# Optimization experiments

Hardware: AMD Instinct MI355X
Metric: run time of the kernel (lower is better)

The kernel has to match this reference:

```python
import jax, jax.numpy as jnp
import numpy as np

B, S, D, H, DOUT = 4, 2048, 1024, 4, 1024


def setup_inputs() -> dict:
    key = jax.random.key(0)
    ks = jax.random.split(key, 11)
    x = jax.random.normal(ks[0], (B, S, D), dtype=jnp.float32)
    phase = jax.random.normal(ks[1], (H, D), dtype=jnp.float32) * 0.02
    sc = 1.0 / np.sqrt(D)
    Wq = jax.random.normal(ks[2], (D, H * D), dtype=jnp.float32) * sc
    bq = jnp.zeros((H * D,), dtype=jnp.float32)
    Wk = jax.random.normal(ks[3], (D, H * D), dtype=jnp.float32) * sc
    bk = jnp.zeros((H * D,), dtype=jnp.float32)
    Wv = jax.random.normal(ks[4], (D, H * D), dtype=jnp.float32) * sc
    bv = jnp.zeros((H * D,), dtype=jnp.float32)
    Wo = jax.random.normal(ks[5], (H * D, DOUT), dtype=jnp.float32) / np.sqrt(H * D)
    bo = jnp.zeros((DOUT,), dtype=jnp.float32)
    return {"x": x, "phase": phase, "Wq": Wq, "bq": bq, "Wk": Wk, "bk": bk,
            "Wv": Wv, "bv": bv, "Wo": Wo, "bo": bo}


def reference(x, phase, Wq, bq, Wk, bk, Wv, bv, Wo, bo):
    b, s, d = x.shape
    h = phase.shape[0]
    q = (x @ Wq + bq).reshape(b, s, h, d)  # [B,S,H,D]
    k = (x @ Wk + bk).reshape(b, s, h, d)
    v = (x @ Wv + bv).reshape(b, s, h, d)
    # q *= e^{i phase}; k *= e^{-i phase}; scores = Re(q @ k^T) over last dim.
    # Re( e^{i p1} e^{-i p2} ) = cos(p1)cos(p2) + sin(p1)sin(p2), so use real pairs.
    c, sn = jnp.cos(phase), jnp.sin(phase)  # [H,D]
    qr, qi = q * c, q * sn
    kr, ki = k * c, k * sn
    scale = 1.0 / np.sqrt(d)
    # per-position head-vs-head scores: [B,S,H,H]
    scores = (jnp.einsum('bshd,bsgd->bshg', qr, kr)
              + jnp.einsum('bshd,bsgd->bshg', qi, ki)) * scale
    attn = jax.nn.softmax(scores, axis=-1)  # dropout is identity in eval
    out = jnp.einsum('bshg,bsgd->bshd', attn, v)  # [B,S,H,D]
    # replicate torch: transpose(1,2) -> [B,H,S,D] then view [B,S,H*D]
    out = jnp.swapaxes(out, 1, 2).reshape(b, s, h * d)
    return out @ Wo + bo
```

## Files before the change

### kernel.cpp

```cpp
#include <hip/hip_runtime.h>
#include <hip/hip_bf16.h>
#include <stdint.h>

#define DEVI __device__ __forceinline__

using f32x4  = __attribute__((ext_vector_type(4))) float;
using bf16x8 = __attribute__((ext_vector_type(8))) short;

DEVI ushort f2bf(float f) {
  union { float f; uint32_t u; } v; v.f = f;
  uint32_t u = v.u;
  uint32_t r = (u + 0x7fffu + ((u >> 16) & 1u)) >> 16;
  return (ushort)r;
}
DEVI float bf2f(ushort h) {
  union { uint32_t u; float f; } v; v.u = ((uint32_t)h) << 16;
  return v.f;
}

__global__ void k_cast_bf16(const float* __restrict__ in, ushort* __restrict__ out, int n8) {
  int i = blockIdx.x * blockDim.x + threadIdx.x;
  if (i >= n8) return;
  const float4* in4 = reinterpret_cast<const float4*>(in);
  float4 a = in4[i * 2], b = in4[i * 2 + 1];
  uint4 o;
  o.x = (uint32_t)f2bf(a.x) | ((uint32_t)f2bf(a.y) << 16);
  o.y = (uint32_t)f2bf(a.z) | ((uint32_t)f2bf(a.w) << 16);
  o.z = (uint32_t)f2bf(b.x) | ((uint32_t)f2bf(b.y) << 16);
  o.w = (uint32_t)f2bf(b.z) | ((uint32_t)f2bf(b.w) << 16);
  reinterpret_cast<uint4*>(out)[i] = o;
}

__global__ __launch_bounds__(256)
void k_transpose_cast(const float* __restrict__ in, ushort* __restrict__ out, int R, int C) {
  __shared__ float tile[64][65];
  int c0 = blockIdx.x * 64, r0 = blockIdx.y * 64;
  int t = threadIdx.x, tr = t >> 6, tc = t & 63;
#pragma unroll
  for (int i = 0; i < 16; ++i) {
    int r = i * 4 + tr;
    tile[r][tc] = in[(size_t)(r0 + r) * C + c0 + tc];
  }
  __syncthreads();
#pragma unroll
  for (int i = 0; i < 16; ++i) {
    int rr = i * 4 + tr;
    out[(size_t)(c0 + rr) * R + r0 + tc] = f2bf(tile[tc][rr]);
  }
}

__global__ void k_phase(const float* __restrict__ p, float* __restrict__ c,
                        float* __restrict__ s, int n) {
  int i = blockIdx.x * blockDim.x + threadIdx.x;
  if (i < n) { float v = p[i]; c[i] = cosf(v); s[i] = sinf(v); }
}

__global__ void k_concat3(const float* __restrict__ a, const float* __restrict__ b,
                          const float* __restrict__ c, float* __restrict__ o, int n) {
  int i = blockIdx.x * blockDim.x + threadIdx.x;
  if (i < n) { o[i] = a[i]; o[i + n] = b[i]; o[i + 2 * n] = c[i]; }
}

DEVI void glds16(const ushort* g, ushort* l) {
  __builtin_amdgcn_global_load_lds(
      (const __attribute__((address_space(1))) void*)g,
      (__attribute__((address_space(3))) void*)l, 16, 0, 0);
}

template <typename OutT>
__global__ __launch_bounds__(512, 2)
void k_gemm256(const ushort* __restrict__ A, const ushort* __restrict__ Bt,
               const float* __restrict__ bias, OutT* __restrict__ C,
               int M, int N, int K) {
  __shared__ ushort lds[3 * 16384];

  int nbx = N >> 8;
  int nwg = gridDim.x, orig = blockIdx.x;
  int q = nwg >> 3, r8 = nwg & 7;
  int xcd = orig & 7, idx = orig >> 3;
  int swz = (xcd < r8 ? xcd * (q + 1) : r8 * (q + 1) + (xcd - r8) * q) + idx;
  int bm = swz / nbx, bn = swz % nbx;

  int t = threadIdx.x;
  int lane = t & 63, wid = t >> 6;
  int wm = wid >> 2, wn = wid & 3;
  int fr = lane & 15, fq = lane >> 4;
  int spR = fq ^ ((fr >> 1) & 3);

  int rl  = t >> 2;
  int spW = (t & 3) ^ ((rl >> 1) & 3);
  const ushort* aS0 = A  + (size_t)(bm * 256 + rl) * K + spW * 8;
  const ushort* aS1 = aS0 + (size_t)128 * K;
  const ushort* bS0 = Bt + (size_t)(bn * 256 + rl) * K + spW * 8;
  const ushort* bS1 = bS0 + (size_t)128 * K;
  ushort* ldsw = lds + wid * 512;

  f32x4 acc[8][4] = {};
  int NT = K >> 5;

  glds16(aS0,      ldsw);
  glds16(aS1,      ldsw + 4096);
  glds16(bS0,      ldsw + 8192);
  glds16(bS1,      ldsw + 12288);
  glds16(aS0 + 32, ldsw + 16384);
  glds16(aS1 + 32, ldsw + 16384 + 4096);
  glds16(bS0 + 32, ldsw + 16384 + 8192);
  glds16(bS1 + 32, ldsw + 16384 + 12288);
  asm volatile("s_waitcnt vmcnt(4)" ::: "memory");
  __builtin_amdgcn_s_barrier();
  __builtin_amdgcn_sched_barrier(0);

  int iA0 = (wm * 128 + fr) * 4 + spR;
  int iB0 = (wn * 64 + fr) * 4 + spR;

  for (int kt = 0; kt < NT; ++kt) {
    if (kt + 2 < NT) {
      ushort* lb = lds + ((kt + 2) % 3) * 16384 + wid * 512;
      int ko = (kt + 2) * 32;
      glds16(aS0 + ko, lb);
      glds16(aS1 + ko, lb + 4096);
      glds16(bS0 + ko, lb + 8192);
      glds16(bS1 + ko, lb + 12288);
    }
    const bf16x8* Av = reinterpret_cast<const bf16x8*>(lds + (kt % 3) * 16384);
    const bf16x8* Bv = Av + 1024;

    bf16x8 bfr[4];
#pragma unroll
    for (int nt = 0; nt < 4; ++nt) bfr[nt] = Bv[iB0 + nt * 64];

#pragma unroll
    for (int mi = 0; mi < 2; ++mi) {
      bf16x8 af[4];
#pragma unroll
      for (int m4 = 0; m4 < 4; ++m4) af[m4] = Av[iA0 + (mi * 4 + m4) * 64];
      __builtin_amdgcn_s_setprio(1);
#pragma unroll
      for (int m4 = 0; m4 < 4; ++m4)
#pragma unroll
        for (int nt = 0; nt < 4; ++nt)
          acc[mi * 4 + m4][nt] =
              __builtin_amdgcn_mfma_f32_16x16x32_bf16(af[m4], bfr[nt], acc[mi * 4 + m4][nt], 0, 0, 0);
      __builtin_amdgcn_s_setprio(0);
    }

    if (kt + 1 < NT) {
      if (kt + 2 < NT) { asm volatile("s_waitcnt vmcnt(4)" ::: "memory"); }
      else             { asm volatile("s_waitcnt vmcnt(0)" ::: "memory"); }
      __builtin_amdgcn_s_barrier();
      __builtin_amdgcn_sched_barrier(0);
    }
  }

#pragma unroll
  for (int mt = 0; mt < 8; ++mt)
#pragma unroll
    for (int nt = 0; nt < 4; ++nt) {
      int col = bn * 256 + wn * 64 + nt * 16 + fr;
      float bb = bias[col];
#pragma unroll
      for (int i = 0; i < 4; ++i) {
        int row = bm * 256 + wm * 128 + mt * 16 + fq * 4 + i;
        float v = acc[mt][nt][i] + bb;
        size_t off = (size_t)row * N + col;
        if constexpr (sizeof(OutT) == 2) C[off] = f2bf(v);
        else                             C[off] = v;
      }
    }
}

template <typename OutT>
__global__ __launch_bounds__(256)
void k_gemm_bt(const ushort* __restrict__ A, const ushort* __restrict__ Bt,
               const float* __restrict__ bias, OutT* __restrict__ C,
               int M, int N, int K) {
  __shared__ ushort As[128 * 32];
  __shared__ ushort Bs[128 * 32];

  int nbx = N >> 7;
  int nwg = gridDim.x;
  int wg  = blockIdx.x;
  int swz = ((nwg & 7) == 0) ? ((wg & 7) * (nwg >> 3) + (wg >> 3)) : wg;
  int bm = swz / nbx, bn = swz % nbx;

  int t = threadIdx.x;
  int lane = t & 63, wid = t >> 6;
  int wr = wid >> 1, wc = wid & 1;
  int fr = lane & 15, fq = lane >> 4;

  f32x4 acc[4][4] = {};

  const ushort* a_src = A  + (size_t)(bm * 128 + (t >> 2)) * K + (t & 3) * 8;
  const ushort* b_src = Bt + (size_t)(bn * 128 + (t >> 2)) * K + (t & 3) * 8;
  ushort* As_w = (ushort*)((char*)As + wid * 1024);
  ushort* Bs_w = (ushort*)((char*)Bs + wid * 1024);

  const bf16x8* As_v = reinterpret_cast<const bf16x8*>(As);
  const bf16x8* Bs_v = reinterpret_cast<const bf16x8*>(Bs);

  for (int k0 = 0; k0 < K; k0 += 32) {
    glds16(a_src + k0,                  As_w);
    glds16(a_src + k0 + (size_t)64 * K, (ushort*)((char*)As_w + 4096));
    glds16(b_src + k0,                  Bs_w);
    glds16(b_src + k0 + (size_t)64 * K, (ushort*)((char*)Bs_w + 4096));
    __syncthreads();

    bf16x8 af[4], bg[4];
#pragma unroll
    for (int mt = 0; mt < 4; ++mt)
      af[mt] = As_v[(wr * 64 + mt * 16 + fr) * 4 + fq];
#pragma unroll
    for (int nt = 0; nt < 4; ++nt)
      bg[nt] = Bs_v[(wc * 64 + nt * 16 + fr) * 4 + fq];
#pragma unroll
    for (int mt = 0; mt < 4; ++mt)
#pragma unroll
      for (int nt = 0; nt < 4; ++nt)
        acc[mt][nt] = __builtin_amdgcn_mfma_f32_16x16x32_bf16(af[mt], bg[nt], acc[mt][nt], 0, 0, 0);
    __syncthreads();
  }

#pragma unroll
  for (int mt = 0; mt < 4; ++mt)
#pragma unroll
    for (int nt = 0; nt < 4; ++nt) {
      int col = bn * 128 + wc * 64 + nt * 16 + fr;
      float bb = bias[col];
#pragma unroll
      for (int i = 0; i < 4; ++i) {
        int row = bm * 128 + wr * 64 + mt * 16 + fq * 4 + i;
        float v = acc[mt][nt][i] + bb;
        size_t off = (size_t)row * N + col;
        if constexpr (sizeof(OutT) == 2) C[off] = f2bf(v);
        else                             C[off] = v;
      }
    }
}

__global__ __launch_bounds__(256)
void k_attn(const ushort* __restrict__ QKV, const float* __restrict__ ct,
            const float* __restrict__ st, ushort* __restrict__ Y) {
  int p = blockIdx.x;
  int t = threadIdx.x;
  int lane = t & 63, wid = t >> 6;
  int d0 = t * 4;
  __shared__ float wsc[4][16];

  float q[4][4], k[4][4], v[4][4], c[4][4], s[4][4];
  const ushort* base = QKV + (size_t)p * 12288 + d0;
#pragma unroll
  for (int h = 0; h < 4; ++h) {
    ushort4 uq = *reinterpret_cast<const ushort4*>(base + h * 1024);
    ushort4 uk = *reinterpret_cast<const ushort4*>(base + 4096 + h * 1024);
    ushort4 uv = *reinterpret_cast<const ushort4*>(base + 8192 + h * 1024);
    q[h][0] = bf2f(uq.x); q[h][1] = bf2f(uq.y); q[h][2] = bf2f(uq.z); q[h][3] = bf2f(uq.w);
    k[h][0] = bf2f(uk.x); k[h][1] = bf2f(uk.y); k[h][2] = bf2f(uk.z); k[h][3] = bf2f(uk.w);
    v[h][0] = bf2f(uv.x); v[h][1] = bf2f(uv.y); v[h][2] = bf2f(uv.z); v[h][3] = bf2f(uv.w);
    float4 fc = *reinterpret_cast<const float4*>(ct + h * 1024 + d0);
    float4 fs = *reinterpret_cast<const float4*>(st + h * 1024 + d0);
    c[h][0] = fc.x; c[h][1] = fc.y; c[h][2] = fc.z; c[h][3] = fc.w;
    s[h][0] = fs.x; s[h][1] = fs.y; s[h][2] = fs.z; s[h][3] = fs.w;
  }
  float qr[4][4], qi[4][4], kr[4][4], ki[4][4];
#pragma unroll
  for (int h = 0; h < 4; ++h)
#pragma unroll
    for (int dd = 0; dd < 4; ++dd) {
      qr[h][dd] = q[h][dd] * c[h][dd];
      qi[h][dd] = q[h][dd] * s[h][dd];
      kr[h][dd] = k[h][dd] * c[h][dd];
      ki[h][dd] = k[h][dd] * s[h][dd];
    }
  float sc[16];
#pragma unroll
  for (int h = 0; h < 4; ++h)
#pragma unroll
    for (int g = 0; g < 4; ++g) {
      float a = 0.f;
#pragma unroll
      for (int dd = 0; dd < 4; ++dd)
        a += qr[h][dd] * kr[g][dd] + qi[h][dd] * ki[g][dd];
      sc[h * 4 + g] = a;
    }
#pragma unroll
  for (int j = 0; j < 16; ++j) {
    float x = sc[j];
    for (int off = 32; off; off >>= 1) x += __shfl_xor(x, off, 64);
    sc[j] = x;
  }
  if (lane == 0) {
#pragma unroll
    for (int j = 0; j < 16; ++j) wsc[wid][j] = sc[j];
  }
  __syncthreads();
  float fsc[16];
#pragma unroll
  for (int j = 0; j < 16; ++j)
    fsc[j] = (wsc[0][j] + wsc[1][j] + wsc[2][j] + wsc[3][j]) * 0.03125f;

  float attn[4][4];
#pragma unroll
  for (int h = 0; h < 4; ++h) {
    float m = fmaxf(fmaxf(fsc[h * 4 + 0], fsc[h * 4 + 1]), fmaxf(fsc[h * 4 + 2], fsc[h * 4 + 3]));
    float e0 = __expf(fsc[h * 4 + 0] - m), e1 = __expf(fsc[h * 4 + 1] - m);
    float e2 = __expf(fsc[h * 4 + 2] - m), e3 = __expf(fsc[h * 4 + 3] - m);
    float inv = 1.f / (e0 + e1 + e2 + e3);
    attn[h][0] = e0 * inv; attn[h][1] = e1 * inv; attn[h][2] = e2 * inv; attn[h][3] = e3 * inv;
  }
  int bl = p >> 11, ss = p & 2047;
#pragma unroll
  for (int h = 0; h < 4; ++h) {
    float o[4];
#pragma unroll
    for (int dd = 0; dd < 4; ++dd)
      o[dd] = attn[h][0] * v[0][dd] + attn[h][1] * v[1][dd] +
              attn[h][2] * v[2][dd] + attn[h][3] * v[3][dd];
    ushort4 ov;
    ov.x = f2bf(o[0]); ov.y = f2bf(o[1]); ov.z = f2bf(o[2]); ov.w = f2bf(o[3]);
    *reinterpret_cast<ushort4*>(Y + ((size_t)(bl * 4 + h) * 2048 + ss) * 1024 + d0) = ov;
  }
}

extern "C" void kernel_launch(void* const* d_in, const int* in_sizes, int n_in,
                              void* d_out, int out_size, void* d_ws, size_t ws_size,
                              hipStream_t stream) {
  const float* x  = (const float*)d_in[0];
  const float* ph = (const float*)d_in[1];
  const float* Wq = (const float*)d_in[2];
  const float* bq = (const float*)d_in[3];
  const float* Wk = (const float*)d_in[4];
  const float* bk = (const float*)d_in[5];
  const float* Wv = (const float*)d_in[6];
  const float* bv = (const float*)d_in[7];
  const float* Wo = (const float*)d_in[8];
  const float* bo = (const float*)d_in[9];
  float* out = (float*)d_out;

  const int B = 4, S = 2048, D = 1024, H = 4;
  const int M = B * S;
  const int HD = H * D;
  const int N3 = 3 * HD;

  const size_t fixed = (size_t)M * D * 2
                     + (size_t)N3 * D * 2
                     + (size_t)D * HD * 2
                     + (size_t)2 * HD * 4
                     + (size_t)N3 * 4;
  int NC; bool full_y;
  if      (ws_size >= fixed + (size_t)M     * N3 * 2 + (size_t)M * HD * 2) { NC = 1; full_y = true; }
  else if (ws_size >= fixed + (size_t)(M/2) * N3 * 2 + (size_t)M * HD * 2) { NC = 2; full_y = true; }
  else if (ws_size >= fixed + (size_t)(M/4) * N3 * 2 + (size_t)M * HD * 2) { NC = 4; full_y = true; }
  else                                                                      { NC = 4; full_y = false; }
  const int Mc = M / NC;

  char* w = (char*)d_ws;
  ushort* Xb    = (ushort*)w; w += (size_t)M * D * 2;
  ushort* WqkvT = (ushort*)w; w += (size_t)N3 * D * 2;
  ushort* WoT   = (ushort*)w; w += (size_t)D * HD * 2;
  float*  ct    = (float*)w;  w += (size_t)HD * 4;
  float*  st    = (float*)w;  w += (size_t)HD * 4;
  float*  bqkv  = (float*)w;  w += (size_t)N3 * 4;
  ushort* QKVc  = (ushort*)w; w += (size_t)Mc * N3 * 2;
  ushort* Yb    = (ushort*)w; w += (size_t)(full_y ? M : Mc) * HD * 2;

  k_cast_bf16<<<(M * D / 8 + 255) / 256, 256, 0, stream>>>(x, Xb, M * D / 8);
  k_transpose_cast<<<dim3(HD / 64, D / 64), 256, 0, stream>>>(Wq, WqkvT,                    D, HD);
  k_transpose_cast<<<dim3(HD / 64, D / 64), 256, 0, stream>>>(Wk, WqkvT + (size_t)HD * D,   D, HD);
  k_transpose_cast<<<dim3(HD / 64, D / 64), 256, 0, stream>>>(Wv, WqkvT + (size_t)2*HD*D,   D, HD);
  k_transpose_cast<<<dim3(D / 64, HD / 64), 256, 0, stream>>>(Wo, WoT, HD, D);
  k_phase<<<(HD + 255) / 256, 256, 0, stream>>>(ph, ct, st, HD);
  k_concat3<<<(HD + 255) / 256, 256, 0, stream>>>(bq, bk, bv, bqkv, HD);

  for (int c = 0; c < NC; ++c) {
    const ushort* Ac = Xb + (size_t)c * Mc * D;
    k_gemm256<ushort><<<(Mc / 256) * (N3 / 256), 512, 0, stream>>>(
        Ac, WqkvT, bqkv, QKVc, Mc, N3, D);
    ushort* Yc = full_y ? (Yb + (size_t)c * Mc * HD) : Yb;
    k_attn<<<Mc, 256, 0, stream>>>(QKVc, ct, st, Yc);
    if (!full_y) {
      k_gemm_bt<float><<<(Mc / 128) * (D / 128), 256, 0, stream>>>(
          Yc, WoT, bo, out + (size_t)c * Mc * D, Mc, D, HD);
    }
  }
  if (full_y) {
    k_gemm_bt<float><<<(M / 128) * (D / 128), 256, 0, stream>>>(Yb, WoT, bo, out, M, D, HD);
  }
}
```

Measured before the change: 440.2 us.

## Replace output GEMM with triple-buffered 256x128 pipelined kernel and remap QKV tiles

The simple 128x128 output-projection GEMM, which did a load-sync-compute-sync loop, is replaced with a 256x128 tile kernel using 512 threads. It triple-buffers LDS via direct global-to-LDS loads with swizzled addressing, uses explicit vmcnt waits and s_setprio around the MFMAs, and prefetches two k-steps ahead. The QKV GEMM also gets a new XCD-aware block mapping that gives each XCD a contiguous band of N columns for better L2 reuse of weights. The cost is more LDS and registers per block and a more fragile hand-scheduled pipeline.

```diff
diff --git a/kernel.cpp b/kernel.cpp
--- a/kernel.cpp
+++ b/kernel.cpp
@@ -76,10 +76,17 @@
 
   int nbx = N >> 8;
   int nwg = gridDim.x, orig = blockIdx.x;
-  int q = nwg >> 3, r8 = nwg & 7;
-  int xcd = orig & 7, idx = orig >> 3;
-  int swz = (xcd < r8 ? xcd * (q + 1) : r8 * (q + 1) + (xcd - r8) * q) + idx;
-  int bm = swz / nbx, bn = swz % nbx;
+  int bm, bn;
+  if ((nbx & 7) == 0 && nbx >= 16 && (nwg & 7) == 0) {
+    int xcd = orig & 7, idx = orig >> 3, sw2 = nbx >> 3;
+    bm = idx / sw2;
+    bn = xcd * sw2 + idx % sw2;
+  } else {
+    int q = nwg >> 3, r8 = nwg & 7;
+    int xcd = orig & 7, idx = orig >> 3;
+    int swz = (xcd < r8 ? xcd * (q + 1) : r8 * (q + 1) + (xcd - r8) * q) + idx;
+    bm = swz / nbx; bn = swz % nbx;
+  }
 
   int t = threadIdx.x;
   int lane = t & 63, wid = t >> 6;
@@ -170,66 +177,90 @@
 }
 
 template <typename OutT>
-__global__ __launch_bounds__(256)
-void k_gemm_bt(const ushort* __restrict__ A, const ushort* __restrict__ Bt,
-               const float* __restrict__ bias, OutT* __restrict__ C,
-               int M, int N, int K) {
-  __shared__ ushort As[128 * 32];
-  __shared__ ushort Bs[128 * 32];
+__global__ __launch_bounds__(512, 2)
+void k_gemm_n128(const ushort* __restrict__ A, const ushort* __restrict__ Bt,
+                 const float* __restrict__ bias, OutT* __restrict__ C,
+                 int M, int N, int K) {
+  __shared__ ushort lds[3 * 12288];
 
   int nbx = N >> 7;
-  int nwg = gridDim.x;
-  int wg  = blockIdx.x;
-  int swz = ((nwg & 7) == 0) ? ((wg & 7) * (nwg >> 3) + (wg >> 3)) : wg;
+  int nwg = gridDim.x, orig = blockIdx.x;
+  int q = nwg >> 3, r8 = nwg & 7;
+  int xcd = orig & 7, idx = orig >> 3;
+  int swz = (xcd < r8 ? xcd * (q + 1) : r8 * (q + 1) + (xcd - r8) * q) + idx;
   int bm = swz / nbx, bn = swz % nbx;
 
   int t = threadIdx.x;
   int lane = t & 63, wid = t >> 6;
-  int wr = wid >> 1, wc = wid & 1;
+  int wm = wid >> 1, wn = wid & 1;
   int fr = lane & 15, fq = lane >> 4;
+  int spR = fq ^ ((fr >> 1) & 3);
+
+  int rl  = t >> 2;
+  int spW = (t & 3) ^ ((rl >> 1) & 3);
+  const ushort* aS0 = A  + (size_t)(bm * 256 + rl) * K + spW * 8;
+  const ushort* aS1 = aS0 + (size_t)128 * K;
+  const ushort* bS0 = Bt + (size_t)(bn * 128 + rl) * K + spW * 8;
+  ushort* ldsw = lds + wid * 512;
 
   f32x4 acc[4][4] = {};
-
-  const ushort* a_src = A  + (size_t)(bm * 128 + (t >> 2)) * K + (t & 3) * 8;
-  const ushort* b_src = Bt + (size_t)(bn * 128 + (t >> 2)) * K + (t & 3) * 8;
-  ushort* As_w = (ushort*)((char*)As + wid * 1024);
-  ushort* Bs_w = (ushort*)((char*)Bs + wid * 1024);
-
-  const bf16x8* As_v = reinterpret_cast<const bf16x8*>(As);
-  const bf16x8* Bs_v = reinterpret_cast<const bf16x8*>(Bs);
-
-  for (int k0 = 0; k0 < K; k0 += 32) {
-    glds16(a_src + k0,                  As_w);
-    glds16(a_src + k0 + (size_t)64 * K, (ushort*)((char*)As_w + 4096));
-    glds16(b_src + k0,                  Bs_w);
-    glds16(b_src + k0 + (size_t)64 * K, (ushort*)((char*)Bs_w + 4096));
-    __syncthreads();
-
-    bf16x8 af[4], bg[4];
-#pragma unroll
-    for (int mt = 0; mt < 4; ++mt)
-      af[mt] = As_v[(wr * 64 + mt * 16 + fr) * 4 + fq];
-#pragma unroll
-    for (int nt = 0; nt < 4; ++nt)
-      bg[nt] = Bs_v[(wc * 64 + nt * 16 + fr) * 4 + fq];
-#pragma unroll
-    for (int mt = 0; mt < 4; ++mt)
+  int NT = K >> 5;
+
+  glds16(aS0,      ldsw);
+  glds16(aS1,      ldsw + 4096);
+  glds16(bS0,      ldsw + 8192);
+  glds16(aS0 + 32, ldsw + 12288);
+  glds16(aS1 + 32, ldsw + 12288 + 4096);
+  glds16(bS0 + 32, ldsw + 12288 + 8192);
+  asm volatile("s_waitcnt vmcnt(3)" ::: "memory");
+  __builtin_amdgcn_s_barrier();
+  __builtin_amdgcn_sched_barrier(0);
+
+  int iA0 = (wm * 64 + fr) * 4 + spR;
+  int iB0 = (wn * 64 + fr) * 4 + spR;
+
+  for (int kt = 0; kt < NT; ++kt) {
+    if (kt + 2 < NT) {
+      ushort* lb = lds + ((kt + 2) % 3) * 12288 + wid * 512;
+      int ko = (kt + 2) * 32;
+      glds16(aS0 + ko, lb);
+      glds16(aS1 + ko, lb + 4096);
+      glds16(bS0 + ko, lb + 8192);
+    }
+    const bf16x8* Av = reinterpret_cast<const bf16x8*>(lds + (kt % 3) * 12288);
+    const bf16x8* Bv = Av + 1024;
+
+    bf16x8 bfr[4], af[4];
+#pragma unroll
+    for (int nt = 0; nt < 4; ++nt) bfr[nt] = Bv[iB0 + nt * 64];
+#pragma unroll
+    for (int m4 = 0; m4 < 4; ++m4) af[m4] = Av[iA0 + m4 * 64];
+    __builtin_amdgcn_s_setprio(1);
+#pragma unroll
+    for (int m4 = 0; m4 < 4; ++m4)
 #pragma unroll
       for (int nt = 0; nt < 4; ++nt)
-        acc[mt][nt] = __builtin_amdgcn_mfma_f32_16x16x32_bf16(af[mt], bg[nt], acc[mt][nt], 0, 0, 0);
-    __syncthreads();
-  }
-
-#pragma unroll
-  for (int mt = 0; mt < 4; ++mt)
+        acc[m4][nt] = __builtin_amdgcn_mfma_f32_16x16x32_bf16(af[m4], bfr[nt], acc[m4][nt], 0, 0, 0);
+    __builtin_amdgcn_s_setprio(0);
+
+    if (kt + 1 < NT) {
+      if (kt + 2 < NT) { asm volatile("s_waitcnt vmcnt(3)" ::: "memory"); }
+      else             { asm volatile("s_waitcnt vmcnt(0)" ::: "memory"); }
+      __builtin_amdgcn_s_barrier();
+      __builtin_amdgcn_sched_barrier(0);
+    }
+  }
+
+#pragma unroll
+  for (int m4 = 0; m4 < 4; ++m4)
 #pragma unroll
     for (int nt = 0; nt < 4; ++nt) {
-      int col = bn * 128 + wc * 64 + nt * 16 + fr;
+      int col = bn * 128 + wn * 64 + nt * 16 + fr;
       float bb = bias[col];
 #pragma unroll
       for (int i = 0; i < 4; ++i) {
-        int row = bm * 128 + wr * 64 + mt * 16 + fq * 4 + i;
-        float v = acc[mt][nt][i] + bb;
+        int row = bm * 256 + wm * 64 + m4 * 16 + fq * 4 + i;
+        float v = acc[m4][nt][i] + bb;
         size_t off = (size_t)row * N + col;
         if constexpr (sizeof(OutT) == 2) C[off] = f2bf(v);
         else                             C[off] = v;
@@ -378,11 +409,11 @@
     ushort* Yc = full_y ? (Yb + (size_t)c * Mc * HD) : Yb;
     k_attn<<<Mc, 256, 0, stream>>>(QKVc, ct, st, Yc);
     if (!full_y) {
-      k_gemm_bt<float><<<(Mc / 128) * (D / 128), 256, 0, stream>>>(
+      k_gemm_n128<float><<<(Mc / 256) * (D / 128), 512, 0, stream>>>(
           Yc, WoT, bo, out + (size_t)c * Mc * D, Mc, D, HD);
     }
   }
   if (full_y) {
-    k_gemm_bt<float><<<(M / 128) * (D / 128), 256, 0, stream>>>(Yb, WoT, bo, out, M, D, HD);
-  }
-}
+    k_gemm_n128<float><<<(M / 256) * (D / 128), 512, 0, stream>>>(Yb, WoT, bo, out, M, D, HD);
+  }
+}
```

Measured after the change: 395.8 us. 10.1% less time.
